# Kernel tuning notes

Hardware: AMD Instinct MI355X
Metric: run time of the kernel (lower is better)

Reference implementation:

```python
import jax, jax.numpy as jnp
from jax import lax
import numpy as np

NUM_Q, DIM_S, SIZE_M = 13523, 128, 64
B, T = 64, 200

def setup_inputs() -> dict:
    key = jax.random.key(0)
    ks = jax.random.split(key, 16)
    def kn(k, shape, fan_in):
        # kaiming_normal_ (fan_in, relu gain sqrt(2))
        return jax.random.normal(k, shape, jnp.float32) * np.sqrt(2.0 / fan_in)
    return {
        "q": jax.random.randint(ks[0], (B, T), 0, NUM_Q),
        "r": jax.random.randint(ks[1], (B, T), 0, 2),
        "k_emb": jax.random.normal(ks[2], (NUM_Q, DIM_S), jnp.float32),
        "v_emb": jax.random.normal(ks[3], (2 * NUM_Q, DIM_S), jnp.float32),
        "Mk": kn(ks[4], (SIZE_M, DIM_S), DIM_S),
        "Mv0": kn(ks[5], (SIZE_M, DIM_S), DIM_S),
        "f_W": jax.random.normal(ks[6], (DIM_S, 2 * DIM_S), jnp.float32) / np.sqrt(2 * DIM_S),
        "f_b": jnp.zeros((DIM_S,), jnp.float32),
        "p_W": jax.random.normal(ks[7], (1, DIM_S), jnp.float32) / np.sqrt(DIM_S),
        "p_b": jnp.zeros((1,), jnp.float32),
        "e_W": jax.random.normal(ks[8], (DIM_S, DIM_S), jnp.float32) / np.sqrt(DIM_S),
        "e_b": jnp.zeros((DIM_S,), jnp.float32),
        "a_W": jax.random.normal(ks[9], (DIM_S, DIM_S), jnp.float32) / np.sqrt(DIM_S),
        "a_b": jnp.zeros((DIM_S,), jnp.float32),
    }

def reference(q, r, k_emb, v_emb, Mk, Mv0, f_W, f_b, p_W, p_b, e_W, e_b, a_W, a_b):
    num_q = k_emb.shape[0]
    x = q + num_q * r                       # [B,T]
    k = k_emb[q]                            # [B,T,D]
    v = v_emb[x]                            # [B,T,D]
    w = jax.nn.softmax(jnp.einsum('btd,md->btm', k, Mk), axis=-1)  # [B,T,M]
    e = jax.nn.sigmoid(v @ e_W.T + e_b)     # [B,T,D]
    a = jnp.tanh(v @ a_W.T + a_b)           # [B,T,D]
    batch = q.shape[0]
    Mv_init = jnp.broadcast_to(Mv0, (batch,) + Mv0.shape)  # [B,M,D]

    def step(Mvt, inp):
        wt, et, at = inp  # [B,M],[B,D],[B,D]
        we = wt[:, :, None]  # [B,M,1]
        Mvt = Mvt * (1.0 - we * et[:, None, :]) + we * at[:, None, :]
        return Mvt, Mvt

    _, Mv_seq = lax.scan(step, Mv_init,
                         (w.transpose(1, 0, 2), e.transpose(1, 0, 2), a.transpose(1, 0, 2)))
    # Mv: [B, T+1, M, D], index t holds memory BEFORE write at step t
    Mv = jnp.concatenate([Mv_init[None], Mv_seq], axis=0).transpose(1, 0, 2, 3)
    read = jnp.einsum('btm,btmd->btd', w, Mv[:, :-1])  # read pre-update memory
    f = jnp.tanh(jnp.concatenate([read, k], axis=-1) @ f_W.T + f_b)
    p = jax.nn.sigmoid(f @ p_W.T + p_b).squeeze(-1)    # [B,T]
    return p, Mv
```

## Files before the change

kernel.cpp:

```cpp
#include <hip/hip_runtime.h>
#include <cstdint>
#include <cstddef>

#define B_   64
#define T_   200
#define NQ_  13523
#define NTOK (B_*T_)

#define O_MKT  0
#define O_EWT  8192
#define O_AWT  24576
#define O_FWT  40960
#define O_W    73728
#define O_EV   892928
#define O_AV   2531328
#define O_KF   4169728
#define O_PART 5808128

#define TOKA 32
#define LSTR 36

__device__ __forceinline__ float sigmoidf_(float x){ return 1.f/(1.f + __expf(-x)); }

__global__ __launch_bounds__(256) void k_prep(const float* __restrict__ Mk,
    const float* __restrict__ eW, const float* __restrict__ aW,
    const float* __restrict__ fW, float* __restrict__ ws)
{
  int i = blockIdx.x*256 + threadIdx.x;
  if (i < 8192){  int j = i>>6, m = i&63;  ws[O_MKT+i] = Mk[m*128 + j]; }
  if (i < 16384){ int j = i>>7, d = i&127; ws[O_EWT+i] = eW[d*128 + j];
                                           ws[O_AWT+i] = aW[d*128 + j]; }
  if (i < 32768){ int c = i>>7, d = i&127; ws[O_FWT+i] = fW[d*256 + c]; }
}

__global__ __launch_bounds__(256) void k_embed(const int* __restrict__ q,
    const int* __restrict__ r, const float* __restrict__ kE,
    const float* __restrict__ vE, const float* __restrict__ eb,
    const float* __restrict__ ab, float* __restrict__ ws)
{
  __shared__ float Kt[128*LSTR];
  __shared__ float Vt[128*LSTR];
  __shared__ int qx[2*TOKA];
  const int tid = threadIdx.x;
  const int it0 = blockIdx.x * TOKA;

  if (tid < TOKA){
    int qq = q[it0+tid];
    qx[tid]      = qq;
    qx[TOKA+tid] = qq + NQ_*r[it0+tid];
  }
  __syncthreads();

  {
    const int j  = tid & 127;
    const int wg = tid >> 7;
    #pragma unroll
    for (int rr=0; rr<4; ++rr){
      const int i0 = rr*8 + wg*4;
      float4 kv, vv;
      kv.x = kE[(size_t)qx[i0+0]*128 + j];
      kv.y = kE[(size_t)qx[i0+1]*128 + j];
      kv.z = kE[(size_t)qx[i0+2]*128 + j];
      kv.w = kE[(size_t)qx[i0+3]*128 + j];
      vv.x = vE[(size_t)qx[TOKA+i0+0]*128 + j];
      vv.y = vE[(size_t)qx[TOKA+i0+1]*128 + j];
      vv.z = vE[(size_t)qx[TOKA+i0+2]*128 + j];
      vv.w = vE[(size_t)qx[TOKA+i0+3]*128 + j];
      *(float4*)&Kt[j*LSTR + i0] = kv;
      *(float4*)&Vt[j*LSTR + i0] = vv;
    }
  }
  __syncthreads();

  const int lane = tid & 63;
  const int wv   = tid >> 6;

  {
    float acc[8] = {0,0,0,0,0,0,0,0};
    #pragma unroll 4
    for (int j=0;j<128;++j){
      float mk  = ws[O_MKT + j*64 + lane];
      float4 k0 = *(const float4*)&Kt[j*LSTR + wv*8];
      float4 k1 = *(const float4*)&Kt[j*LSTR + wv*8 + 4];
      acc[0] = fmaf(k0.x, mk, acc[0]);
      acc[1] = fmaf(k0.y, mk, acc[1]);
      acc[2] = fmaf(k0.z, mk, acc[2]);
      acc[3] = fmaf(k0.w, mk, acc[3]);
      acc[4] = fmaf(k1.x, mk, acc[4]);
      acc[5] = fmaf(k1.y, mk, acc[5]);
      acc[6] = fmaf(k1.z, mk, acc[6]);
      acc[7] = fmaf(k1.w, mk, acc[7]);
    }
    #pragma unroll
    for (int ii=0;ii<8;++ii){
      float x = acc[ii];
      float mx = x;
      #pragma unroll
      for (int off=32; off>0; off>>=1) mx = fmaxf(mx, __shfl_xor(mx, off));
      float ex = __expf(x - mx);
      float sm = ex;
      #pragma unroll
      for (int off=32; off>0; off>>=1) sm += __shfl_xor(sm, off);
      ws[O_W + (size_t)(it0 + wv*8 + ii)*64 + lane] = ex/sm;
    }
  }

  {
    const int d0 = lane, d1 = lane + 64;
    float aE0[8]={0},aE1[8]={0},aA0[8]={0},aA1[8]={0},aK0[8]={0},aK1[8]={0};
    #pragma unroll 2
    for (int j=0;j<128;++j){
      float we0 = ws[O_EWT + j*128 + d0];
      float we1 = ws[O_EWT + j*128 + d1];
      float wa0 = ws[O_AWT + j*128 + d0];
      float wa1 = ws[O_AWT + j*128 + d1];
      float wf0 = ws[O_FWT + (128+j)*128 + d0];
      float wf1 = ws[O_FWT + (128+j)*128 + d1];
      float4 v0 = *(const float4*)&Vt[j*LSTR + wv*8];
      float4 v1 = *(const float4*)&Vt[j*LSTR + wv*8 + 4];
      float4 k0 = *(const float4*)&Kt[j*LSTR + wv*8];
      float4 k1 = *(const float4*)&Kt[j*LSTR + wv*8 + 4];
      float vv[8] = {v0.x,v0.y,v0.z,v0.w,v1.x,v1.y,v1.z,v1.w};
      float kk[8] = {k0.x,k0.y,k0.z,k0.w,k1.x,k1.y,k1.z,k1.w};
      #pragma unroll
      for (int ii=0;ii<8;++ii){
        aE0[ii] = fmaf(vv[ii], we0, aE0[ii]);
        aE1[ii] = fmaf(vv[ii], we1, aE1[ii]);
        aA0[ii] = fmaf(vv[ii], wa0, aA0[ii]);
        aA1[ii] = fmaf(vv[ii], wa1, aA1[ii]);
        aK0[ii] = fmaf(kk[ii], wf0, aK0[ii]);
        aK1[ii] = fmaf(kk[ii], wf1, aK1[ii]);
      }
    }
    const float eb0 = eb[d0], eb1 = eb[d1];
    const float ab0 = ab[d0], ab1 = ab[d1];
    #pragma unroll
    for (int ii=0;ii<8;++ii){
      size_t it = (size_t)(it0 + wv*8 + ii);
      ws[O_EV + it*128 + d0] = sigmoidf_(aE0[ii] + eb0);
      ws[O_EV + it*128 + d1] = sigmoidf_(aE1[ii] + eb1);
      ws[O_AV + it*128 + d0] = tanhf(aA0[ii] + ab0);
      ws[O_AV + it*128 + d1] = tanhf(aA1[ii] + ab1);
      ws[O_KF + it*128 + d0] = aK0[ii];
      ws[O_KF + it*128 + d1] = aK1[ii];
    }
  }
}

__global__ __launch_bounds__(256) void k_scan(const float* __restrict__ Mv0,
    float* __restrict__ ws, float* __restrict__ out)
{
  __shared__ float red[256];
  const int tid = threadIdx.x;
  const int b  = blockIdx.x >> 2;
  const int c  = blockIdx.x & 3;
  const int d  = tid & 127;
  const int mg = tid >> 7;
  const int m0 = c*16 + mg*8;

  float s[8];
  float* mv = out + NTOK + (size_t)b*201*64*128;
  #pragma unroll
  for (int j=0;j<8;++j){
    s[j] = Mv0[(m0+j)*128 + d];
    __builtin_nontemporal_store(s[j], &mv[(size_t)(m0+j)*128 + d]);
  }
  const float* wp = ws + O_W  + (size_t)b*T_*64  + m0;
  const float* ep = ws + O_EV + (size_t)b*T_*128 + d;
  const float* ap = ws + O_AV + (size_t)b*T_*128 + d;
  float* pp = ws + O_PART + (size_t)c*NTOK*128 + (size_t)b*T_*128 + tid;

  float4 wA = *(const float4*)(wp);
  float4 wB = *(const float4*)(wp+4);
  float ec = ep[0];
  float ac = ap[0];
  for (int t=0; t<T_; ++t){
    const int tn = (t < T_-1) ? t+1 : t;
    float4 nA = *(const float4*)(wp + (size_t)tn*64);
    float4 nB = *(const float4*)(wp + (size_t)tn*64 + 4);
    float ne = ep[(size_t)tn*128];
    float na = ap[(size_t)tn*128];

    float w[8] = {wA.x,wA.y,wA.z,wA.w,wB.x,wB.y,wB.z,wB.w};
    float racc = 0.f;
    #pragma unroll
    for (int j=0;j<8;++j) racc = fmaf(w[j], s[j], racc);
    #pragma unroll
    for (int j=0;j<8;++j){
      float we = w[j]*ec;
      s[j] = fmaf(-we, s[j], fmaf(w[j], ac, s[j]));
    }
    float* mvt = mv + (size_t)(t+1)*64*128;
    #pragma unroll
    for (int j=0;j<8;++j)
      __builtin_nontemporal_store(s[j], &mvt[(size_t)(m0+j)*128 + d]);

    red[tid] = racc;
    __syncthreads();
    if (tid < 128) pp[(size_t)t*128] = red[tid] + red[tid+128];
    __syncthreads();

    wA=nA; wB=nB; ec=ne; ac=na;
  }
}

__global__ __launch_bounds__(256) void k_out(const float* __restrict__ ws,
    const float* __restrict__ fb, const float* __restrict__ pW,
    const float* __restrict__ pb, float* __restrict__ out)
{
  __shared__ float Rt[128*LSTR];
  const int tid = threadIdx.x;
  const int it0 = blockIdx.x * TOKA;
  {
    const int j  = tid & 127;
    const int wg = tid >> 7;
    const float* P = ws + O_PART;
    #pragma unroll
    for (int rr=0; rr<4; ++rr){
      const int i0 = rr*8 + wg*4;
      float v4[4];
      #pragma unroll
      for (int ii=0;ii<4;++ii){
        size_t base = (size_t)(it0+i0+ii)*128 + j;
        v4[ii] = P[base] + P[(size_t)NTOK*128 + base]
               + P[2*(size_t)NTOK*128 + base] + P[3*(size_t)NTOK*128 + base];
      }
      *(float4*)&Rt[j*LSTR + i0] = make_float4(v4[0],v4[1],v4[2],v4[3]);
    }
  }
  __syncthreads();
  const int lane = tid & 63, wv = tid >> 6;
  const int d0 = lane, d1 = lane + 64;
  float a0[8]={0,0,0,0,0,0,0,0}, a1[8]={0,0,0,0,0,0,0,0};
  #pragma unroll 2
  for (int j=0;j<128;++j){
    float w0 = ws[O_FWT + j*128 + d0];
    float w1 = ws[O_FWT + j*128 + d1];
    float4 r0 = *(const float4*)&Rt[j*LSTR + wv*8];
    float4 r1 = *(const float4*)&Rt[j*LSTR + wv*8 + 4];
    float rv[8] = {r0.x,r0.y,r0.z,r0.w,r1.x,r1.y,r1.z,r1.w};
    #pragma unroll
    for (int ii=0;ii<8;++ii){
      a0[ii] = fmaf(rv[ii], w0, a0[ii]);
      a1[ii] = fmaf(rv[ii], w1, a1[ii]);
    }
  }
  const float fb0 = fb[d0], fb1 = fb[d1];
  const float pw0 = pW[d0], pw1 = pW[d1];
  #pragma unroll
  for (int ii=0;ii<8;++ii){
    size_t it = (size_t)(it0 + wv*8 + ii);
    float f0 = tanhf(a0[ii] + ws[O_KF + it*128 + d0] + fb0);
    float f1 = tanhf(a1[ii] + ws[O_KF + it*128 + d1] + fb1);
    float part = fmaf(f0, pw0, f1*pw1);
    #pragma unroll
    for (int off=32; off>0; off>>=1) part += __shfl_xor(part, off);
    if (lane == 0) out[it] = sigmoidf_(part + pb[0]);
  }
}

extern "C" void kernel_launch(void* const* d_in, const int* in_sizes, int n_in,
                              void* d_out, int out_size, void* d_ws, size_t ws_size,
                              hipStream_t stream)
{
  const int*   q   = (const int*)d_in[0];
  const int*   r   = (const int*)d_in[1];
  const float* kE  = (const float*)d_in[2];
  const float* vE  = (const float*)d_in[3];
  const float* Mk  = (const float*)d_in[4];
  const float* Mv0 = (const float*)d_in[5];
  const float* fW  = (const float*)d_in[6];
  const float* fb  = (const float*)d_in[7];
  const float* pW  = (const float*)d_in[8];
  const float* pb  = (const float*)d_in[9];
  const float* eW  = (const float*)d_in[10];
  const float* eb  = (const float*)d_in[11];
  const float* aW  = (const float*)d_in[12];
  const float* ab  = (const float*)d_in[13];
  float* out = (float*)d_out;
  float* ws  = (float*)d_ws;

  k_prep <<<128, 256, 0, stream>>>(Mk, eW, aW, fW, ws);
  k_embed<<<NTOK/TOKA, 256, 0, stream>>>(q, r, kE, vE, eb, ab, ws);
  k_scan <<<256, 256, 0, stream>>>(Mv0, ws, out);
  k_out  <<<NTOK/TOKA, 256, 0, stream>>>(ws, fb, pW, pb, out);
}
```

Baseline: 532.3 us.

## Split memory scan across eight chunks per batch and batch partial-read reductions

The recurrent scan now splits each batch's 64 memory rows across 8 blocks instead of 4, with 4 rows per thread, which doubles the block count to raise occupancy and latency hiding on the serial time loop. Read partials are buffered in registers and reduced through shared memory once every 8 steps, cutting the two block-wide barriers per step to two per eight steps. In exchange the partial-read workspace doubles and the output kernel must sum 8 partials per element, adding global traffic. It also relies on the workspace being large enough for 8 partial planes.

Result: no change. 538.6 us (+1.2%).

```diff
diff --git a/kernel.cpp b/kernel.cpp
--- a/kernel.cpp
+++ b/kernel.cpp
@@ -17,6 +17,7 @@
 #define O_KF   4169728
 #define O_PART 5808128
 
+#define NCH  8
 #define TOKA 32
 #define LSTR 36
 
@@ -150,57 +151,67 @@
 __global__ __launch_bounds__(256) void k_scan(const float* __restrict__ Mv0,
     float* __restrict__ ws, float* __restrict__ out)
 {
-  __shared__ float red[256];
-  const int tid = threadIdx.x;
-  const int b  = blockIdx.x >> 2;
-  const int c  = blockIdx.x & 3;
-  const int d  = tid & 127;
-  const int mg = tid >> 7;
-  const int m0 = c*16 + mg*8;
-
-  float s[8];
+  __shared__ float red[2*8*128];
+  const int tid  = threadIdx.x;
+  const int b    = blockIdx.x >> 3;
+  const int c    = blockIdx.x & 7;
+  const int d    = tid & 127;
+  const int mrow = tid >> 7;
+  const int m0   = c*8 + mrow*4;
+
+  float s[4];
   float* mv = out + NTOK + (size_t)b*201*64*128;
   #pragma unroll
-  for (int j=0;j<8;++j){
+  for (int j=0;j<4;++j){
     s[j] = Mv0[(m0+j)*128 + d];
     __builtin_nontemporal_store(s[j], &mv[(size_t)(m0+j)*128 + d]);
   }
   const float* wp = ws + O_W  + (size_t)b*T_*64  + m0;
   const float* ep = ws + O_EV + (size_t)b*T_*128 + d;
   const float* ap = ws + O_AV + (size_t)b*T_*128 + d;
-  float* pp = ws + O_PART + (size_t)c*NTOK*128 + (size_t)b*T_*128 + tid;
-
+  float* pp = ws + O_PART + (size_t)c*NTOK*128 + (size_t)b*T_*128;
+
+  float racc8[8];
   float4 wA = *(const float4*)(wp);
-  float4 wB = *(const float4*)(wp+4);
   float ec = ep[0];
   float ac = ap[0];
   for (int t=0; t<T_; ++t){
     const int tn = (t < T_-1) ? t+1 : t;
     float4 nA = *(const float4*)(wp + (size_t)tn*64);
-    float4 nB = *(const float4*)(wp + (size_t)tn*64 + 4);
     float ne = ep[(size_t)tn*128];
     float na = ap[(size_t)tn*128];
 
-    float w[8] = {wA.x,wA.y,wA.z,wA.w,wB.x,wB.y,wB.z,wB.w};
+    float w[4] = {wA.x,wA.y,wA.z,wA.w};
     float racc = 0.f;
     #pragma unroll
-    for (int j=0;j<8;++j) racc = fmaf(w[j], s[j], racc);
-    #pragma unroll
-    for (int j=0;j<8;++j){
+    for (int j=0;j<4;++j) racc = fmaf(w[j], s[j], racc);
+    racc8[t & 7] = racc;
+    #pragma unroll
+    for (int j=0;j<4;++j){
       float we = w[j]*ec;
       s[j] = fmaf(-we, s[j], fmaf(w[j], ac, s[j]));
     }
     float* mvt = mv + (size_t)(t+1)*64*128;
     #pragma unroll
-    for (int j=0;j<8;++j)
+    for (int j=0;j<4;++j)
       __builtin_nontemporal_store(s[j], &mvt[(size_t)(m0+j)*128 + d]);
 
-    red[tid] = racc;
-    __syncthreads();
-    if (tid < 128) pp[(size_t)t*128] = red[tid] + red[tid+128];
-    __syncthreads();
-
-    wA=nA; wB=nB; ec=ne; ac=na;
+    if ((t & 7) == 7){
+      #pragma unroll
+      for (int i=0;i<8;++i) red[(mrow*8 + i)*128 + d] = racc8[i];
+      __syncthreads();
+      const int t0 = t - 7;
+      #pragma unroll
+      for (int k=0;k<4;++k){
+        int idx = tid + k*256;
+        int i  = idx >> 7;
+        int dd = idx & 127;
+        pp[(size_t)(t0+i)*128 + dd] = red[i*128 + dd] + red[(8+i)*128 + dd];
+      }
+      __syncthreads();
+    }
+
+    wA=nA; ec=ne; ac=na;
   }
 }
 
@@ -222,8 +233,10 @@
       #pragma unroll
       for (int ii=0;ii<4;++ii){
         size_t base = (size_t)(it0+i0+ii)*128 + j;
-        v4[ii] = P[base] + P[(size_t)NTOK*128 + base]
-               + P[2*(size_t)NTOK*128 + base] + P[3*(size_t)NTOK*128 + base];
+        float sum = 0.f;
+        #pragma unroll
+        for (int p=0;p<NCH;++p) sum += P[(size_t)p*NTOK*128 + base];
+        v4[ii] = sum;
       }
       *(float4*)&Rt[j*LSTR + i0] = make_float4(v4[0],v4[1],v4[2],v4[3]);
     }
@@ -282,6 +295,6 @@
 
   k_prep <<<128, 256, 0, stream>>>(Mk, eW, aW, fW, ws);
   k_embed<<<NTOK/TOKA, 256, 0, stream>>>(q, r, kE, vE, eb, ab, ws);
-  k_scan <<<256, 256, 0, stream>>>(Mv0, ws, out);
+  k_scan <<<B_*NCH, 256, 0, stream>>>(Mv0, ws, out);
   k_out  <<<NTOK/TOKA, 256, 0, stream>>>(ws, fb, pW, pb, out);
 }
```
